# Kernel optimization log

Hardware: AMD Instinct MI355X
Metric: run time of the kernel (lower is better)

The kernel has to match this reference:

```python
import jax, jax.numpy as jnp
import numpy as np

N_MELS = 80
FORMANT_START, FORMANT_END = 10, 50
W_L1, W_DELTA, W_DELTA2, W_SC, W_BAND, FORMANT_W = 1.0, 0.5, 0.25, 0.5, 1.0, 2.0
EPS = 1e-8


def _masked_mean(x, mask):
    # mask broadcasts to x's shape; count = sum of the broadcast mask
    n = jnp.maximum(jnp.sum(jnp.broadcast_to(mask, x.shape)), 1.0)
    return jnp.sum(x * mask) / n


def setup_inputs() -> dict:
    key = jax.random.key(0)
    k1, k2, k3 = jax.random.split(key, 3)
    B, T, D = 64, 4000, N_MELS
    pred_mel = jax.random.normal(k1, (B, T, D), dtype=jnp.float32)
    target_mel = jax.random.normal(k2, (B, T, D), dtype=jnp.float32)
    lengths = jax.random.randint(k3, (B,), T // 2, T + 1)
    mel_mask = (jnp.arange(T)[None, :] < lengths[:, None]).astype(jnp.float32)
    band_weights = jnp.ones((D,), dtype=jnp.float32).at[FORMANT_START:FORMANT_END].set(FORMANT_W)
    return {"pred_mel": pred_mel, "target_mel": target_mel, "mel_mask": mel_mask,
            "band_weights": band_weights}


def reference(pred_mel, target_mel, mel_mask, band_weights):
    mask3 = mel_mask[:, :, None]                      # (B,T,1)

    l1 = jnp.abs(pred_mel - target_mel)               # (B,T,D)
    l1_loss = _masked_mean(l1, mask3)

    # 1st-order deltas
    dp = pred_mel[:, 1:] - pred_mel[:, :-1]
    dt = target_mel[:, 1:] - target_mel[:, :-1]
    dmask = (mel_mask[:, 1:] * mel_mask[:, :-1])[:, :, None]
    delta_loss = _masked_mean(jnp.abs(dp - dt), dmask)

    # 2nd-order deltas
    d2p = dp[:, 1:] - dp[:, :-1]
    d2t = dt[:, 1:] - dt[:, :-1]
    d2mask = (mel_mask[:, 2:] * mel_mask[:, 1:-1] * mel_mask[:, :-2])[:, :, None]
    delta2_loss = _masked_mean(jnp.abs(d2p - d2t), d2mask)

    # spectral convergence
    diff = (pred_mel - target_mel) * mask3
    tgt_m = target_mel * mask3
    n = jnp.maximum(jnp.sum(jnp.broadcast_to(mask3, pred_mel.shape)), 1.0)
    sc_num = jnp.sqrt(jnp.sum(diff * diff) / n)
    sc_den = jnp.maximum(jnp.sqrt(jnp.sum(tgt_m * tgt_m) / n), EPS)
    sc_loss = sc_num / sc_den

    # band-weighted L1
    w = band_weights[None, None, :]
    band_loss = _masked_mean(l1 * w, mask3) / jnp.mean(band_weights)

    # energy (per-frame mean over mel bins)
    e_l1 = jnp.abs(pred_mel.mean(axis=-1) - target_mel.mean(axis=-1))  # (B,T)
    energy_loss = _masked_mean(e_l1, mel_mask)

    return (W_L1 * l1_loss + W_DELTA * delta_loss + W_DELTA2 * delta2_loss
            + W_SC * sc_loss + W_BAND * band_loss + 0.5 * energy_loss)
```

## Files before the change

kernel.cpp:

```cpp
#include <hip/hip_runtime.h>
#include <math.h>

#define D_MELS 80
#define T_DIM  4000
#define NQ     10
#define NTHR   256
#define RPI    14


__global__ __launch_bounds__(NTHR) void mel_loss_main(
    const float* __restrict__ pred, const float* __restrict__ tgt,
    const float* __restrict__ mask,
    float* __restrict__ partial, int BT, int Jtot, int K, int nblk)
{
    const int tid  = threadIdx.x;
    const int lane = tid & 63;
    const int qtr  = lane & 3;
    const int rw   = lane >> 2;
    const int gw   = blockIdx.x * (NTHR / 64) + (tid >> 6);

    const float4* p4 = (const float4*)pred;
    const float4* q4 = (const float4*)tgt;

    const int lsrc4 = (lane - 4) & 63;
    const int lsrc8 = (lane - 8) & 63;

    float4 sel0 = make_float4(0.f, 0.f, 0.f, 0.f);
    float4 sel3 = make_float4(0.f, 0.f, 0.f, 0.f);
    if (qtr == 2)      { sel0.z = 1.f; sel0.w = 1.f; }
    else if (qtr == 3) { sel0.x = 1.f; sel0.y = 1.f; sel0.z = 1.f; sel0.w = 1.f; }
    if (qtr == 0)      { sel3.x = 1.f; sel3.y = 1.f; }

    float v_l1 = 0.f, v_band = 0.f, v_diff2 = 0.f, v_tgt2 = 0.f, v_energy = 0.f;
    float v_m = 0.f, v_d = 0.f, v_dm = 0.f, v_d2 = 0.f, v_d2m = 0.f;

    const int j0 = gw * K;
    const int j1 = (j0 + K < Jtot) ? (j0 + K) : Jtot;

    for (int j = j0; j < j1; ++j) {
        const int r = j * RPI - 2 + rw;
        int rload = r;
        if (rload < 0) rload = 0;
        if (rload >= BT) rload = BT - 1;
        const int t = rload % T_DIM;

        const float4* pr = p4 + (size_t)rload * (D_MELS / 4) + qtr;
        const float4* qr = q4 + (size_t)rload * (D_MELS / 4) + qtr;

        float mload = mask[rload];
        float m1 = __shfl(mload, lsrc4, 64);
        float m2 = __shfl(mload, lsrc8, 64);

        const bool contrib = (rw >= 2) && (r < BT);
        float mt   = contrib ? mload : 0.f;
        float dmv  = (t >= 1) ? mt * m1 : 0.f;
        float d2mv = (t >= 2) ? dmv * m2 : 0.f;

        float l1r = 0.f, frr = 0.f, sqr = 0.f, t2r = 0.f, er = 0.f, dr = 0.f, d2r = 0.f;

        #pragma unroll
        for (int k = 0; k < 5; ++k) {
            float4 p = pr[4 * k];
            float4 q = qr[4 * k];
            float e0 = p.x - q.x, e1 = p.y - q.y, e2 = p.z - q.z, e3 = p.w - q.w;

            float f0 = __shfl(e0, lsrc4, 64);
            float f1 = __shfl(e1, lsrc4, 64);
            float f2 = __shfl(e2, lsrc4, 64);
            float f3 = __shfl(e3, lsrc4, 64);
            float g0 = __shfl(e0, lsrc8, 64);
            float g1 = __shfl(e1, lsrc8, 64);
            float g2 = __shfl(e2, lsrc8, 64);
            float g3 = __shfl(e3, lsrc8, 64);

            float a0 = fabsf(e0), a1 = fabsf(e1), a2 = fabsf(e2), a3 = fabsf(e3);
            float ak = a0 + a1 + a2 + a3;
            l1r += ak;
            if (k == 1 || k == 2)      frr += ak;
            else if (k == 0)           frr += a0 * sel0.x + a1 * sel0.y + a2 * sel0.z + a3 * sel0.w;
            else if (k == 3)           frr += a0 * sel3.x + a1 * sel3.y + a2 * sel3.z + a3 * sel3.w;

            sqr += e0 * e0 + e1 * e1 + e2 * e2 + e3 * e3;
            t2r += q.x * q.x + q.y * q.y + q.z * q.z + q.w * q.w;
            er  += e0 + e1 + e2 + e3;
            dr  += fabsf(e0 - f0) + fabsf(e1 - f1) + fabsf(e2 - f2) + fabsf(e3 - f3);
            d2r += fabsf(e0 - 2.f * f0 + g0) + fabsf(e1 - 2.f * f1 + g1)
                 + fabsf(e2 - 2.f * f2 + g2) + fabsf(e3 - 2.f * f3 + g3);
        }

        v_l1    += l1r * mt;
        v_band  += (l1r + frr) * mt;
        v_diff2 += sqr * mt;
        v_tgt2  += t2r * mt;
        v_d     += dr * dmv;
        v_d2    += d2r * d2mv;

        er += __shfl_xor(er, 1, 64);
        er += __shfl_xor(er, 2, 64);
        if (qtr == 0) {
            v_energy += fabsf(er) * mt;
            v_m   += mt;
            v_dm  += dmv;
            v_d2m += d2mv;
        }
    }

    float vals[NQ] = {v_l1, v_band, v_diff2, v_tgt2, v_energy,
                      v_m, v_d, v_dm, v_d2, v_d2m};
    #pragma unroll
    for (int q = 0; q < NQ; ++q) {
        float v = vals[q];
        #pragma unroll
        for (int off = 32; off > 0; off >>= 1)
            v += __shfl_down(v, off, 64);
        vals[q] = v;
    }
    __shared__ float red[NTHR / 64][NQ];
    int wave = tid >> 6;
    if (lane == 0) {
        #pragma unroll
        for (int q = 0; q < NQ; ++q) red[wave][q] = vals[q];
    }
    __syncthreads();
    if (tid < NQ) {
        float s = 0.f;
        #pragma unroll
        for (int wv2 = 0; wv2 < NTHR / 64; ++wv2) s += red[wv2][tid];
        partial[tid * nblk + blockIdx.x] = s;
    }
}

__global__ __launch_bounds__(640) void mel_loss_finalize(
    const float* __restrict__ partial, const float* __restrict__ w,
    float* __restrict__ out, int nblk)
{
    const int tid = threadIdx.x;
    const int wv  = tid >> 6;
    const int lane = tid & 63;
    __shared__ float fin[NQ];

    float s = 0.f;
    for (int i = lane; i < nblk; i += 64) s += partial[wv * nblk + i];
    #pragma unroll
    for (int off = 32; off > 0; off >>= 1) s += __shfl_down(s, off, 64);
    if (lane == 0 && wv < NQ) fin[wv] = s;
    __syncthreads();

    if (tid == 0) {
        float l1s = fin[0], bands = fin[1], diff2 = fin[2], tgt2 = fin[3];
        float energys = fin[4], ms = fin[5], ds = fin[6], dms = fin[7];
        float d2s = fin[8], d2ms = fin[9];

        float wsum = 0.f;
        for (int d = 0; d < D_MELS; ++d) wsum += w[d];
        float wmean = wsum / (float)D_MELS;

        float n1  = fmaxf(ms   * (float)D_MELS, 1.f);
        float nd  = fmaxf(dms  * (float)D_MELS, 1.f);
        float nd2 = fmaxf(d2ms * (float)D_MELS, 1.f);

        float l1_loss     = l1s / n1;
        float delta_loss  = ds / nd;
        float delta2_loss = d2s / nd2;
        float sc_num = sqrtf(diff2 / n1);
        float sc_den = fmaxf(sqrtf(tgt2 / n1), 1e-8f);
        float sc_loss = sc_num / sc_den;
        float band_loss = (bands / n1) / wmean;
        float energy_loss = (energys / (float)D_MELS) / fmaxf(ms, 1.f);

        out[0] = 1.0f * l1_loss + 0.5f * delta_loss + 0.25f * delta2_loss
               + 0.5f * sc_loss + 1.0f * band_loss + 0.5f * energy_loss;
    }
}

extern "C" void kernel_launch(void* const* d_in, const int* in_sizes, int n_in,
                              void* d_out, int out_size, void* d_ws, size_t ws_size,
                              hipStream_t stream) {
    const float* pred = (const float*)d_in[0];
    const float* tgt  = (const float*)d_in[1];
    const float* mask = (const float*)d_in[2];
    const float* w    = (const float*)d_in[3];
    int BT = in_sizes[2];
    float* partial = (float*)d_ws;

    int Jtot = (BT + RPI - 1) / RPI;
    int K = 2;
    int nwaves = (Jtot + K - 1) / K;
    int grid = (nwaves + (NTHR / 64) - 1) / (NTHR / 64);
    while ((size_t)NQ * (size_t)grid * sizeof(float) > ws_size && K < Jtot) {
        K *= 2;
        nwaves = (Jtot + K - 1) / K;
        grid = (nwaves + (NTHR / 64) - 1) / (NTHR / 64);
    }

    mel_loss_main<<<grid, NTHR, 0, stream>>>(pred, tgt, mask, partial, BT, Jtot, K, grid);
    mel_loss_finalize<<<1, 640, 0, stream>>>(partial, w, (float*)d_out, grid);
}
```

Baseline: 198.3 us.

## Skip loading fully masked row groups and hardcode two groups per wave

```diff
diff --git a/kernel.cpp b/kernel.cpp
--- a/kernel.cpp
+++ b/kernel.cpp
@@ -8,10 +8,10 @@
 #define RPI    14
 
 
-__global__ __launch_bounds__(NTHR) void mel_loss_main(
+__global__ __launch_bounds__(NTHR, 8) void mel_loss_main(
     const float* __restrict__ pred, const float* __restrict__ tgt,
     const float* __restrict__ mask,
-    float* __restrict__ partial, int BT, int Jtot, int K, int nblk)
+    float* __restrict__ partial, int BT, int Jtot, int nblk)
 {
     const int tid  = threadIdx.x;
     const int lane = tid & 63;
@@ -21,40 +21,40 @@
 
     const float4* p4 = (const float4*)pred;
     const float4* q4 = (const float4*)tgt;
-
     const int lsrc4 = (lane - 4) & 63;
     const int lsrc8 = (lane - 8) & 63;
-
-    float4 sel0 = make_float4(0.f, 0.f, 0.f, 0.f);
-    float4 sel3 = make_float4(0.f, 0.f, 0.f, 0.f);
-    if (qtr == 2)      { sel0.z = 1.f; sel0.w = 1.f; }
-    else if (qtr == 3) { sel0.x = 1.f; sel0.y = 1.f; sel0.z = 1.f; sel0.w = 1.f; }
-    if (qtr == 0)      { sel3.x = 1.f; sel3.y = 1.f; }
 
     float v_l1 = 0.f, v_band = 0.f, v_diff2 = 0.f, v_tgt2 = 0.f, v_energy = 0.f;
     float v_m = 0.f, v_d = 0.f, v_dm = 0.f, v_d2 = 0.f, v_d2m = 0.f;
 
-    const int j0 = gw * K;
-    const int j1 = (j0 + K < Jtot) ? (j0 + K) : Jtot;
+    const int j0 = gw * 2;
 
-    for (int j = j0; j < j1; ++j) {
-        const int r = j * RPI - 2 + rw;
-        int rload = r;
-        if (rload < 0) rload = 0;
-        if (rload >= BT) rload = BT - 1;
+    int r0 = j0 * RPI - 2 + rw;
+    int r1 = r0 + RPI;
+    int rl0 = r0 < 0 ? 0 : (r0 >= BT ? BT - 1 : r0);
+    int rl1 = r1 < 0 ? 0 : (r1 >= BT ? BT - 1 : r1);
+
+    float mv0 = (j0     < Jtot) ? mask[rl0] : 0.f;
+    float mv1 = (j0 + 1 < Jtot) ? mask[rl1] : 0.f;
+
+    #pragma unroll
+    for (int s = 0; s < 2; ++s) {
+        const int r     = s ? r1  : r0;
+        const int rload = s ? rl1 : rl0;
+        const float mload = s ? mv1 : mv0;
+
+        if (!__any(mload != 0.0f)) continue;
+
         const int t = rload % T_DIM;
-
         const float4* pr = p4 + (size_t)rload * (D_MELS / 4) + qtr;
         const float4* qr = q4 + (size_t)rload * (D_MELS / 4) + qtr;
 
-        float mload = mask[rload];
-        float m1 = __shfl(mload, lsrc4, 64);
-        float m2 = __shfl(mload, lsrc8, 64);
-
+        const float m1 = __shfl(mload, lsrc4, 64);
+        const float m2 = __shfl(mload, lsrc8, 64);
         const bool contrib = (rw >= 2) && (r < BT);
-        float mt   = contrib ? mload : 0.f;
-        float dmv  = (t >= 1) ? mt * m1 : 0.f;
-        float d2mv = (t >= 2) ? dmv * m2 : 0.f;
+        const float mt   = contrib ? mload : 0.f;
+        const float dmv  = (t >= 1) ? mt * m1 : 0.f;
+        const float d2mv = (t >= 2) ? dmv * m2 : 0.f;
 
         float l1r = 0.f, frr = 0.f, sqr = 0.f, t2r = 0.f, er = 0.f, dr = 0.f, d2r = 0.f;
 
@@ -76,9 +76,9 @@
             float a0 = fabsf(e0), a1 = fabsf(e1), a2 = fabsf(e2), a3 = fabsf(e3);
             float ak = a0 + a1 + a2 + a3;
             l1r += ak;
-            if (k == 1 || k == 2)      frr += ak;
-            else if (k == 0)           frr += a0 * sel0.x + a1 * sel0.y + a2 * sel0.z + a3 * sel0.w;
-            else if (k == 3)           frr += a0 * sel3.x + a1 * sel3.y + a2 * sel3.z + a3 * sel3.w;
+            if (k == 1 || k == 2) frr += ak;
+            else if (k == 0)      frr += (qtr == 2) ? (a2 + a3) : ((qtr == 3) ? ak : 0.f);
+            else if (k == 3)      frr += (qtr == 0) ? (a0 + a1) : 0.f;
 
             sqr += e0 * e0 + e1 * e1 + e2 * e2 + e3 * e3;
             t2r += q.x * q.x + q.y * q.y + q.z * q.z + q.w * q.w;
@@ -184,15 +184,9 @@
     float* partial = (float*)d_ws;
 
     int Jtot = (BT + RPI - 1) / RPI;
-    int K = 2;
-    int nwaves = (Jtot + K - 1) / K;
+    int nwaves = (Jtot + 1) / 2;
     int grid = (nwaves + (NTHR / 64) - 1) / (NTHR / 64);
-    while ((size_t)NQ * (size_t)grid * sizeof(float) > ws_size && K < Jtot) {
-        K *= 2;
-        nwaves = (Jtot + K - 1) / K;
-        grid = (nwaves + (NTHR / 64) - 1) / (NTHR / 64);
-    }
 
-    mel_loss_main<<<grid, NTHR, 0, stream>>>(pred, tgt, mask, partial, BT, Jtot, K, grid);
+    mel_loss_main<<<grid, NTHR, 0, stream>>>(pred, tgt, mask, partial, BT, Jtot, grid);
     mel_loss_finalize<<<1, 640, 0, stream>>>(partial, w, (float*)d_out, grid);
 }
```

After: 204.4 us. 1.03x slower.
